# Optimization experiments

Measured on AMD Instinct MI355X. Metric: run time of the kernel, lower is better.

Reference implementation:

```python
import jax, jax.numpy as jnp
import numpy as np

N_NODES = 50000
N_EDGES = 600000
IN_CH = 128
OUT_CH = 128
HEADS = 1


def setup_inputs() -> dict:
    key = jax.random.key(0)
    ks = jax.random.split(key, 6)
    x = jax.random.normal(ks[0], (N_NODES, IN_CH), dtype=jnp.float32)
    edge_index = jax.random.randint(ks[1], (2, N_EDGES), 0, N_NODES, dtype=jnp.int64)
    weight = jax.random.normal(ks[2], (IN_CH, HEADS * OUT_CH), dtype=jnp.float32) * (1.0 / np.sqrt(IN_CH))
    u = jax.random.normal(ks[3], (IN_CH, HEADS), dtype=jnp.float32) * (1.0 / np.sqrt(IN_CH))
    c = jax.random.normal(ks[4], (HEADS,), dtype=jnp.float32)
    bias = jax.random.normal(ks[5], (OUT_CH,), dtype=jnp.float32) * 0.01
    return {"x": x, "edge_index": edge_index, "weight": weight, "u": u, "c": c, "bias": bias}


def reference(x, edge_index, weight, u, c, bias):
    N = x.shape[0]
    # FeaStConv default add_self_loops=True
    loops = jnp.arange(N, dtype=edge_index.dtype)
    src = jnp.concatenate([edge_index[0], loops])  # x_j (source / neighbor)
    dst = jnp.concatenate([edge_index[1], loops])  # x_i (target / center)
    # per-edge soft assignment over heads: q = softmax((x_j - x_i) @ u + c)
    q = jax.nn.softmax((x[src] - x[dst]) @ u + c, axis=1)          # [E, H]
    xj = (x[src] @ weight).reshape(-1, HEADS, OUT_CH)              # [E, H, F]
    msg = (xj * q[:, :, None]).sum(axis=1)                         # [E, F]
    # mean aggregation over incoming edges at each target node
    agg = jax.ops.segment_sum(msg, dst, num_segments=N)
    cnt = jax.ops.segment_sum(jnp.ones((dst.shape[0],), x.dtype), dst, num_segments=N)
    out = agg / jnp.maximum(cnt, 1.0)[:, None] + bias
    return jax.nn.relu(out)
```

## Files before the change

### kernel.cpp

```cpp
#include <hip/hip_runtime.h>

#define N_NODES 50000
#define N_EDGES 600000
#define CH 128
#define ROWS 32
#define MD 32
#define SPILL_CAP 65536
#define HSTRIDE 136

typedef __attribute__((ext_vector_type(8))) short bf16x8;
typedef __attribute__((ext_vector_type(4))) float f32x4;

__device__ inline unsigned int f2bf(float f) {
    unsigned int b = __float_as_uint(f);
    unsigned int r = b + 0x7fffu + ((b >> 16) & 1u);
    return r >> 16;
}

__device__ inline void acc8(float* a, int4 u) {
    a[0] += __uint_as_float(((unsigned int)u.x) << 16);
    a[1] += __uint_as_float(((unsigned int)u.x) & 0xffff0000u);
    a[2] += __uint_as_float(((unsigned int)u.y) << 16);
    a[3] += __uint_as_float(((unsigned int)u.y) & 0xffff0000u);
    a[4] += __uint_as_float(((unsigned int)u.z) << 16);
    a[5] += __uint_as_float(((unsigned int)u.z) & 0xffff0000u);
    a[6] += __uint_as_float(((unsigned int)u.w) << 16);
    a[7] += __uint_as_float(((unsigned int)u.w) & 0xffff0000u);
}

__global__ __launch_bounds__(256) void k_prep(const float* __restrict__ x,
                                              const float* __restrict__ Wm,
                                              unsigned short* __restrict__ xh,
                                              unsigned short* __restrict__ Wt,
                                              int* __restrict__ deg, int degN,
                                              int* __restrict__ spill_cnt) {
    int i = blockIdx.x * 256 + threadIdx.x;
    const int NX4 = N_NODES * CH / 4;
    if (i < NX4) {
        float4 v = ((const float4*)x)[i];
        ushort4 o;
        o.x = (unsigned short)f2bf(v.x);
        o.y = (unsigned short)f2bf(v.y);
        o.z = (unsigned short)f2bf(v.z);
        o.w = (unsigned short)f2bf(v.w);
        ((ushort4*)xh)[i] = o;
    }
    if (i < degN / 4) ((int4*)deg)[i] = make_int4(0, 0, 0, 0);
    if (i < CH * CH) {
        int n = i >> 7, k = i & 127;
        Wt[n * CH + k] = (unsigned short)f2bf(Wm[k * CH + n]);
    }
    if (i == 0) *spill_cnt = 0;
}

__global__ __launch_bounds__(256) void k_histfill(const int* __restrict__ ei,
                                                  int* __restrict__ deg, int pad,
                                                  int* __restrict__ ell,
                                                  int* __restrict__ spill_cnt,
                                                  int* __restrict__ spill) {
    int idx = blockIdx.x * 256 + threadIdx.x;
    if (idx * 4 >= N_EDGES) return;
    int4 s = ((const int4*)ei)[idx];
    int4 d = ((const int4*)(ei + N_EDGES))[idx];
    #pragma unroll
    for (int q = 0; q < 4; ++q) {
        int src = (q == 0) ? s.x : (q == 1) ? s.y : (q == 2) ? s.z : s.w;
        int dst = (q == 0) ? d.x : (q == 1) ? d.y : (q == 2) ? d.z : d.w;
        int r = atomicAdd(&deg[dst * pad], 1);
        if (r < MD) {
            ell[dst * MD + r] = src;
        } else {
            int p = atomicAdd(spill_cnt, 1);
            if (p < SPILL_CAP) {
                spill[2 * p] = src;
                spill[2 * p + 1] = dst;
            }
        }
    }
}

__global__ __launch_bounds__(256) void k_agg_mfma(
    const unsigned short* __restrict__ xh, const int* __restrict__ deg, int pad,
    const int* __restrict__ ell, const int* __restrict__ spill_cnt,
    const int* __restrict__ spill, const unsigned short* __restrict__ Wt,
    const float* __restrict__ bias, float* __restrict__ out) {
    __shared__ __align__(16) unsigned short HsB[ROWS * HSTRIDE];
    const int t = threadIdx.x;
    const int wv = t >> 6;
    const int lane = t & 63;
    const int quad = lane >> 4;
    const int l16 = lane & 15;
    const int row0 = blockIdx.x * ROWS;
    const int c8 = l16 * 8;

    #pragma unroll
    for (int kk = 0; kk < 2; ++kk) {
        const int ln = wv * 8 + kk * 4 + quad;
        const int n = row0 + ln;
        float a[8] = {0.f, 0.f, 0.f, 0.f, 0.f, 0.f, 0.f, 0.f};
        float inv = 1.0f;
        if (n < N_NODES) {
            acc8(a, *(const int4*)(xh + (size_t)n * CH + c8));
            const int d = deg[n * pad];
            const int dl = (d < MD) ? d : MD;
            const int* cl = ell + (size_t)n * MD;
            int j = 0;
            for (; j + 3 < dl; j += 4) {
                int e0 = cl[j], e1 = cl[j + 1], e2 = cl[j + 2], e3 = cl[j + 3];
                int4 u0 = *(const int4*)(xh + (size_t)e0 * CH + c8);
                int4 u1 = *(const int4*)(xh + (size_t)e1 * CH + c8);
                int4 u2 = *(const int4*)(xh + (size_t)e2 * CH + c8);
                int4 u3 = *(const int4*)(xh + (size_t)e3 * CH + c8);
                acc8(a, u0); acc8(a, u1); acc8(a, u2); acc8(a, u3);
            }
            for (; j < dl; ++j)
                acc8(a, *(const int4*)(xh + (size_t)cl[j] * CH + c8));
            int sc = *spill_cnt;
            if (sc > SPILL_CAP) sc = SPILL_CAP;
            for (int sidx = 0; sidx < sc; ++sidx) {
                if (spill[2 * sidx + 1] == n)
                    acc8(a, *(const int4*)(xh + (size_t)spill[2 * sidx] * CH + c8));
            }
            inv = 1.0f / (float)(d + 1);
        }
        int4 p;
        p.x = (int)(f2bf(a[0] * inv) | (f2bf(a[1] * inv) << 16));
        p.y = (int)(f2bf(a[2] * inv) | (f2bf(a[3] * inv) << 16));
        p.z = (int)(f2bf(a[4] * inv) | (f2bf(a[5] * inv) << 16));
        p.w = (int)(f2bf(a[6] * inv) | (f2bf(a[7] * inv) << 16));
        *(int4*)&HsB[ln * HSTRIDE + c8] = p;
    }
    __syncthreads();

    const int rt = wv >> 1;
    const int cstart = (wv & 1) * 64;
    f32x4 acc[4];
    #pragma unroll
    for (int tt = 0; tt < 4; ++tt) acc[tt] = (f32x4){0.f, 0.f, 0.f, 0.f};

    const unsigned short* hrow = &HsB[(rt * 16 + l16) * HSTRIDE + quad * 8];
    #pragma unroll
    for (int ks = 0; ks < 4; ++ks) {
        bf16x8 af = *(const bf16x8*)(hrow + ks * 32);
        #pragma unroll
        for (int tt = 0; tt < 4; ++tt) {
            const int ncol = cstart + tt * 16 + l16;
            bf16x8 bf = *(const bf16x8*)(Wt + (size_t)ncol * CH + ks * 32 + quad * 8);
            acc[tt] = __builtin_amdgcn_mfma_f32_16x16x32_bf16(af, bf, acc[tt], 0, 0, 0);
        }
    }

    #pragma unroll
    for (int tt = 0; tt < 4; ++tt) {
        const int ncol = cstart + tt * 16 + l16;
        const float bv = bias[ncol];
        #pragma unroll
        for (int r = 0; r < 4; ++r) {
            const int row = row0 + rt * 16 + quad * 4 + r;
            if (row < N_NODES)
                out[(size_t)row * CH + ncol] = fmaxf(acc[tt][r] + bv, 0.f);
        }
    }
}

extern "C" void kernel_launch(void* const* d_in, const int* in_sizes, int n_in,
                              void* d_out, int out_size, void* d_ws, size_t ws_size,
                              hipStream_t stream) {
    const float* x    = (const float*)d_in[0];
    const int*   ei   = (const int*)d_in[1];
    const float* Wm   = (const float*)d_in[2];
    const float* bias = (const float*)d_in[5];
    float* out = (float*)d_out;

    const size_t xh_bytes   = (size_t)N_NODES * CH * 2;
    const size_t wt_bytes   = (size_t)CH * CH * 2;
    const size_t ell_bytes  = (size_t)N_NODES * MD * 4;
    const size_t spill_bytes = (size_t)(1 + 2 * SPILL_CAP) * 4;
    const size_t fixed = xh_bytes + wt_bytes + ell_bytes + spill_bytes;

    int pad = 1;
    if (ws_size >= fixed + (size_t)N_NODES * 32 * 4) pad = 32;
    else if (ws_size >= fixed + (size_t)N_NODES * 8 * 4) pad = 8;
    const int degN = ((N_NODES * pad + 3) / 4) * 4;

    unsigned short* xh = (unsigned short*)d_ws;
    unsigned short* Wt = (unsigned short*)((char*)d_ws + xh_bytes);
    int* ell       = (int*)((char*)d_ws + xh_bytes + wt_bytes);
    int* spill_cnt = ell + (size_t)N_NODES * MD;
    int* spill     = spill_cnt + 1;
    int* deg       = spill + 2 * SPILL_CAP;

    k_prep<<<dim3((N_NODES * CH / 4 + 255) / 256), dim3(256), 0, stream>>>(
        x, Wm, xh, Wt, deg, degN, spill_cnt);
    k_histfill<<<dim3((N_EDGES / 4 + 255) / 256), dim3(256), 0, stream>>>(
        ei, deg, pad, ell, spill_cnt, spill);
    k_agg_mfma<<<dim3((N_NODES + ROWS - 1) / ROWS), dim3(256), 0, stream>>>(
        xh, deg, pad, ell, spill_cnt, spill, Wt, bias, out);
}
```

Measured before the change: 163.5 us.

## Fuse prep and histogram kernels, use 16-bit ELL, interleave two-node gathers

Merges the bf16 conversion and the edge histogram/ELL fill into one launch split by block index, with the degree and spill counters zeroed by a memset. The ELL neighbour list is stored as 16-bit indices to halve index traffic. The aggregation loop now gathers two nodes' neighbours together so more independent loads are in flight, and it skips the spill scan when no edges spilled. The 16-bit indices cannot hold source ids at or above 65536; with 50000 nodes they fit. Running the histogram concurrently with the conversion drops the dependency the old separate launch gave, so it relies on the histogram not reading xh.

```diff
diff --git a/kernel.cpp b/kernel.cpp
--- a/kernel.cpp
+++ b/kernel.cpp
@@ -7,6 +7,8 @@
 #define MD 32
 #define SPILL_CAP 65536
 #define HSTRIDE 136
+#define PREP_BLOCKS 6250
+#define HIST_BLOCKS 586
 
 typedef __attribute__((ext_vector_type(8))) short bf16x8;
 typedef __attribute__((ext_vector_type(4))) float f32x4;
@@ -28,15 +30,16 @@
     a[7] += __uint_as_float(((unsigned int)u.w) & 0xffff0000u);
 }
 
-__global__ __launch_bounds__(256) void k_prep(const float* __restrict__ x,
-                                              const float* __restrict__ Wm,
-                                              unsigned short* __restrict__ xh,
-                                              unsigned short* __restrict__ Wt,
-                                              int* __restrict__ deg, int degN,
-                                              int* __restrict__ spill_cnt) {
-    int i = blockIdx.x * 256 + threadIdx.x;
-    const int NX4 = N_NODES * CH / 4;
-    if (i < NX4) {
+__global__ __launch_bounds__(256) void k_prep_hist(
+    const float* __restrict__ x, const float* __restrict__ Wm,
+    const int* __restrict__ ei, unsigned short* __restrict__ xh,
+    unsigned short* __restrict__ Wt, unsigned short* __restrict__ ellu,
+    int* __restrict__ deg, int pad, int* __restrict__ spill_cnt,
+    int* __restrict__ spill) {
+    const int b = blockIdx.x;
+    const int t = threadIdx.x;
+    if (b < PREP_BLOCKS) {
+        int i = b * 256 + t;
         float4 v = ((const float4*)x)[i];
         ushort4 o;
         o.x = (unsigned short)f2bf(v.x);
@@ -44,36 +47,28 @@
         o.z = (unsigned short)f2bf(v.z);
         o.w = (unsigned short)f2bf(v.w);
         ((ushort4*)xh)[i] = o;
-    }
-    if (i < degN / 4) ((int4*)deg)[i] = make_int4(0, 0, 0, 0);
-    if (i < CH * CH) {
-        int n = i >> 7, k = i & 127;
-        Wt[n * CH + k] = (unsigned short)f2bf(Wm[k * CH + n]);
-    }
-    if (i == 0) *spill_cnt = 0;
-}
-
-__global__ __launch_bounds__(256) void k_histfill(const int* __restrict__ ei,
-                                                  int* __restrict__ deg, int pad,
-                                                  int* __restrict__ ell,
-                                                  int* __restrict__ spill_cnt,
-                                                  int* __restrict__ spill) {
-    int idx = blockIdx.x * 256 + threadIdx.x;
-    if (idx * 4 >= N_EDGES) return;
-    int4 s = ((const int4*)ei)[idx];
-    int4 d = ((const int4*)(ei + N_EDGES))[idx];
-    #pragma unroll
-    for (int q = 0; q < 4; ++q) {
-        int src = (q == 0) ? s.x : (q == 1) ? s.y : (q == 2) ? s.z : s.w;
-        int dst = (q == 0) ? d.x : (q == 1) ? d.y : (q == 2) ? d.z : d.w;
-        int r = atomicAdd(&deg[dst * pad], 1);
-        if (r < MD) {
-            ell[dst * MD + r] = src;
-        } else {
-            int p = atomicAdd(spill_cnt, 1);
-            if (p < SPILL_CAP) {
-                spill[2 * p] = src;
-                spill[2 * p + 1] = dst;
+        if (i < CH * CH) {
+            int n = i >> 7, k = i & 127;
+            Wt[n * CH + k] = (unsigned short)f2bf(Wm[k * CH + n]);
+        }
+    } else {
+        int idx = (b - PREP_BLOCKS) * 256 + t;
+        if (idx * 4 >= N_EDGES) return;
+        int4 s = ((const int4*)ei)[idx];
+        int4 d = ((const int4*)(ei + N_EDGES))[idx];
+        #pragma unroll
+        for (int q = 0; q < 4; ++q) {
+            int src = (q == 0) ? s.x : (q == 1) ? s.y : (q == 2) ? s.z : s.w;
+            int dst = (q == 0) ? d.x : (q == 1) ? d.y : (q == 2) ? d.z : d.w;
+            int r = atomicAdd(&deg[dst * pad], 1);
+            if (r < MD) {
+                ellu[dst * MD + r] = (unsigned short)src;
+            } else {
+                int p = atomicAdd(spill_cnt, 1);
+                if (p < SPILL_CAP) {
+                    spill[2 * p] = src;
+                    spill[2 * p + 1] = dst;
+                }
             }
         }
     }
@@ -81,7 +76,7 @@
 
 __global__ __launch_bounds__(256) void k_agg_mfma(
     const unsigned short* __restrict__ xh, const int* __restrict__ deg, int pad,
-    const int* __restrict__ ell, const int* __restrict__ spill_cnt,
+    const unsigned short* __restrict__ ellu, const int* __restrict__ spill_cnt,
     const int* __restrict__ spill, const unsigned short* __restrict__ Wt,
     const float* __restrict__ bias, float* __restrict__ out) {
     __shared__ __align__(16) unsigned short HsB[ROWS * HSTRIDE];
@@ -93,42 +88,77 @@
     const int row0 = blockIdx.x * ROWS;
     const int c8 = l16 * 8;
 
-    #pragma unroll
-    for (int kk = 0; kk < 2; ++kk) {
-        const int ln = wv * 8 + kk * 4 + quad;
-        const int n = row0 + ln;
-        float a[8] = {0.f, 0.f, 0.f, 0.f, 0.f, 0.f, 0.f, 0.f};
-        float inv = 1.0f;
-        if (n < N_NODES) {
-            acc8(a, *(const int4*)(xh + (size_t)n * CH + c8));
-            const int d = deg[n * pad];
-            const int dl = (d < MD) ? d : MD;
-            const int* cl = ell + (size_t)n * MD;
-            int j = 0;
-            for (; j + 3 < dl; j += 4) {
-                int e0 = cl[j], e1 = cl[j + 1], e2 = cl[j + 2], e3 = cl[j + 3];
-                int4 u0 = *(const int4*)(xh + (size_t)e0 * CH + c8);
-                int4 u1 = *(const int4*)(xh + (size_t)e1 * CH + c8);
-                int4 u2 = *(const int4*)(xh + (size_t)e2 * CH + c8);
-                int4 u3 = *(const int4*)(xh + (size_t)e3 * CH + c8);
-                acc8(a, u0); acc8(a, u1); acc8(a, u2); acc8(a, u3);
-            }
-            for (; j < dl; ++j)
-                acc8(a, *(const int4*)(xh + (size_t)cl[j] * CH + c8));
-            int sc = *spill_cnt;
+    {
+        const int lnA = wv * 8 + quad;
+        const int lnB = lnA + 4;
+        const int nA = row0 + lnA;
+        const int nB = row0 + lnB;
+        float a[8] = {}, bacc[8] = {};
+        int dA = 0, dB = 0;
+        if (nA < N_NODES) {
+            acc8(a, *(const int4*)(xh + (size_t)nA * CH + c8));
+            dA = deg[nA * pad];
+        }
+        if (nB < N_NODES) {
+            acc8(bacc, *(const int4*)(xh + (size_t)nB * CH + c8));
+            dB = deg[nB * pad];
+        }
+        const int dlA = (dA < MD) ? dA : MD;
+        const int dlB = (dB < MD) ? dB : MD;
+        const unsigned short* clA = ellu + (size_t)nA * MD;
+        const unsigned short* clB = ellu + (size_t)nB * MD;
+        const int dmax = (dlA > dlB) ? dlA : dlB;
+
+        for (int j = 0; j < dmax; j += 4) {
+            ushort4 cA = make_ushort4(0, 0, 0, 0), cB = make_ushort4(0, 0, 0, 0);
+            if (j < dlA) cA = *(const ushort4*)(clA + j);
+            if (j < dlB) cB = *(const ushort4*)(clB + j);
+            int4 uA0, uA1, uA2, uA3, uB0, uB1, uB2, uB3;
+            bool pA0 = j + 0 < dlA, pA1 = j + 1 < dlA, pA2 = j + 2 < dlA, pA3 = j + 3 < dlA;
+            bool pB0 = j + 0 < dlB, pB1 = j + 1 < dlB, pB2 = j + 2 < dlB, pB3 = j + 3 < dlB;
+            if (pA0) uA0 = *(const int4*)(xh + (size_t)cA.x * CH + c8);
+            if (pA1) uA1 = *(const int4*)(xh + (size_t)cA.y * CH + c8);
+            if (pA2) uA2 = *(const int4*)(xh + (size_t)cA.z * CH + c8);
+            if (pA3) uA3 = *(const int4*)(xh + (size_t)cA.w * CH + c8);
+            if (pB0) uB0 = *(const int4*)(xh + (size_t)cB.x * CH + c8);
+            if (pB1) uB1 = *(const int4*)(xh + (size_t)cB.y * CH + c8);
+            if (pB2) uB2 = *(const int4*)(xh + (size_t)cB.z * CH + c8);
+            if (pB3) uB3 = *(const int4*)(xh + (size_t)cB.w * CH + c8);
+            if (pA0) acc8(a, uA0);
+            if (pA1) acc8(a, uA1);
+            if (pA2) acc8(a, uA2);
+            if (pA3) acc8(a, uA3);
+            if (pB0) acc8(bacc, uB0);
+            if (pB1) acc8(bacc, uB1);
+            if (pB2) acc8(bacc, uB2);
+            if (pB3) acc8(bacc, uB3);
+        }
+
+        int sc = *spill_cnt;
+        if (sc > 0) {
             if (sc > SPILL_CAP) sc = SPILL_CAP;
             for (int sidx = 0; sidx < sc; ++sidx) {
-                if (spill[2 * sidx + 1] == n)
+                int sdst = spill[2 * sidx + 1];
+                if (sdst == nA)
                     acc8(a, *(const int4*)(xh + (size_t)spill[2 * sidx] * CH + c8));
+                if (sdst == nB)
+                    acc8(bacc, *(const int4*)(xh + (size_t)spill[2 * sidx] * CH + c8));
             }
-            inv = 1.0f / (float)(d + 1);
-        }
+        }
+
+        const float invA = 1.0f / (float)(dA + 1);
+        const float invB = 1.0f / (float)(dB + 1);
         int4 p;
-        p.x = (int)(f2bf(a[0] * inv) | (f2bf(a[1] * inv) << 16));
-        p.y = (int)(f2bf(a[2] * inv) | (f2bf(a[3] * inv) << 16));
-        p.z = (int)(f2bf(a[4] * inv) | (f2bf(a[5] * inv) << 16));
-        p.w = (int)(f2bf(a[6] * inv) | (f2bf(a[7] * inv) << 16));
-        *(int4*)&HsB[ln * HSTRIDE + c8] = p;
+        p.x = (int)(f2bf(a[0] * invA) | (f2bf(a[1] * invA) << 16));
+        p.y = (int)(f2bf(a[2] * invA) | (f2bf(a[3] * invA) << 16));
+        p.z = (int)(f2bf(a[4] * invA) | (f2bf(a[5] * invA) << 16));
+        p.w = (int)(f2bf(a[6] * invA) | (f2bf(a[7] * invA) << 16));
+        *(int4*)&HsB[lnA * HSTRIDE + c8] = p;
+        p.x = (int)(f2bf(bacc[0] * invB) | (f2bf(bacc[1] * invB) << 16));
+        p.y = (int)(f2bf(bacc[2] * invB) | (f2bf(bacc[3] * invB) << 16));
+        p.z = (int)(f2bf(bacc[4] * invB) | (f2bf(bacc[5] * invB) << 16));
+        p.w = (int)(f2bf(bacc[6] * invB) | (f2bf(bacc[7] * invB) << 16));
+        *(int4*)&HsB[lnB * HSTRIDE + c8] = p;
     }
     __syncthreads();
 
@@ -172,9 +202,9 @@
     const float* bias = (const float*)d_in[5];
     float* out = (float*)d_out;
 
-    const size_t xh_bytes   = (size_t)N_NODES * CH * 2;
-    const size_t wt_bytes   = (size_t)CH * CH * 2;
-    const size_t ell_bytes  = (size_t)N_NODES * MD * 4;
+    const size_t xh_bytes  = (size_t)N_NODES * CH * 2;
+    const size_t wt_bytes  = (size_t)CH * CH * 2;
+    const size_t ell_bytes = (size_t)N_NODES * MD * 2;
     const size_t spill_bytes = (size_t)(1 + 2 * SPILL_CAP) * 4;
     const size_t fixed = xh_bytes + wt_bytes + ell_bytes + spill_bytes;
 
@@ -183,17 +213,16 @@
     else if (ws_size >= fixed + (size_t)N_NODES * 8 * 4) pad = 8;
     const int degN = ((N_NODES * pad + 3) / 4) * 4;
 
-    unsigned short* xh = (unsigned short*)d_ws;
-    unsigned short* Wt = (unsigned short*)((char*)d_ws + xh_bytes);
-    int* ell       = (int*)((char*)d_ws + xh_bytes + wt_bytes);
-    int* spill_cnt = ell + (size_t)N_NODES * MD;
+    unsigned short* xh   = (unsigned short*)d_ws;
+    unsigned short* Wt   = (unsigned short*)((char*)d_ws + xh_bytes);
+    unsigned short* ellu = (unsigned short*)((char*)d_ws + xh_bytes + wt_bytes);
+    int* deg       = (int*)((char*)d_ws + xh_bytes + wt_bytes + ell_bytes);
+    int* spill_cnt = deg + degN;
     int* spill     = spill_cnt + 1;
-    int* deg       = spill + 2 * SPILL_CAP;
-
-    k_prep<<<dim3((N_NODES * CH / 4 + 255) / 256), dim3(256), 0, stream>>>(
-        x, Wm, xh, Wt, deg, degN, spill_cnt);
-    k_histfill<<<dim3((N_EDGES / 4 + 255) / 256), dim3(256), 0, stream>>>(
-        ei, deg, pad, ell, spill_cnt, spill);
+
+    hipMemsetAsync(deg, 0, (size_t)degN * 4 + 4, stream);
+    k_prep_hist<<<dim3(PREP_BLOCKS + HIST_BLOCKS), dim3(256), 0, stream>>>(
+        x, Wm, ei, xh, Wt, ellu, deg, pad, spill_cnt, spill);
     k_agg_mfma<<<dim3((N_NODES + ROWS - 1) / ROWS), dim3(256), 0, stream>>>(
-        xh, deg, pad, ell, spill_cnt, spill, Wt, bias, out);
-}
+        xh, deg, pad, ellu, spill_cnt, spill, Wt, bias, out);
+}
```

Measured after the change: 175.4 us. 1.07x slower.

## Merge prep and histogram kernels into one launch and halve aggregation tile rows

Applied to the files above, without the earlier changes.

The bf16 conversion of x and W and the edge-to-ELL histogram fill now run as disjoint block ranges of a single kernel. The degree array and spill counter are zeroed beforehand by one hipMemsetAsync. This removes a kernel boundary and lets the two independent prep phases overlap. The aggregation kernel now handles 16 rows per block, so each wave does one node and a 32-column MFMA slice, which doubles the block count. It also drops bounds checks and skips the spill scan when no edges spilled, at the cost of more per-block reloads of the weight matrix.

```diff
diff --git a/kernel.cpp b/kernel.cpp
--- a/kernel.cpp
+++ b/kernel.cpp
@@ -3,10 +3,12 @@
 #define N_NODES 50000
 #define N_EDGES 600000
 #define CH 128
-#define ROWS 32
+#define ROWS 16
 #define MD 32
 #define SPILL_CAP 65536
 #define HSTRIDE 136
+#define PREP_BLOCKS 6250
+#define HIST_BLOCKS 586
 
 typedef __attribute__((ext_vector_type(8))) short bf16x8;
 typedef __attribute__((ext_vector_type(4))) float f32x4;
@@ -28,15 +30,16 @@
     a[7] += __uint_as_float(((unsigned int)u.w) & 0xffff0000u);
 }
 
-__global__ __launch_bounds__(256) void k_prep(const float* __restrict__ x,
-                                              const float* __restrict__ Wm,
-                                              unsigned short* __restrict__ xh,
-                                              unsigned short* __restrict__ Wt,
-                                              int* __restrict__ deg, int degN,
-                                              int* __restrict__ spill_cnt) {
-    int i = blockIdx.x * 256 + threadIdx.x;
-    const int NX4 = N_NODES * CH / 4;
-    if (i < NX4) {
+__global__ __launch_bounds__(256) void k_prep_hist(
+    const float* __restrict__ x, const float* __restrict__ Wm,
+    const int* __restrict__ ei, unsigned short* __restrict__ xh,
+    unsigned short* __restrict__ Wt, int* __restrict__ ell,
+    int* __restrict__ deg, int pad, int* __restrict__ spill_cnt,
+    int* __restrict__ spill) {
+    const int b = blockIdx.x;
+    const int t = threadIdx.x;
+    if (b < PREP_BLOCKS) {
+        int i = b * 256 + t;
         float4 v = ((const float4*)x)[i];
         ushort4 o;
         o.x = (unsigned short)f2bf(v.x);
@@ -44,36 +47,28 @@
         o.z = (unsigned short)f2bf(v.z);
         o.w = (unsigned short)f2bf(v.w);
         ((ushort4*)xh)[i] = o;
-    }
-    if (i < degN / 4) ((int4*)deg)[i] = make_int4(0, 0, 0, 0);
-    if (i < CH * CH) {
-        int n = i >> 7, k = i & 127;
-        Wt[n * CH + k] = (unsigned short)f2bf(Wm[k * CH + n]);
-    }
-    if (i == 0) *spill_cnt = 0;
-}
-
-__global__ __launch_bounds__(256) void k_histfill(const int* __restrict__ ei,
-                                                  int* __restrict__ deg, int pad,
-                                                  int* __restrict__ ell,
-                                                  int* __restrict__ spill_cnt,
-                                                  int* __restrict__ spill) {
-    int idx = blockIdx.x * 256 + threadIdx.x;
-    if (idx * 4 >= N_EDGES) return;
-    int4 s = ((const int4*)ei)[idx];
-    int4 d = ((const int4*)(ei + N_EDGES))[idx];
-    #pragma unroll
-    for (int q = 0; q < 4; ++q) {
-        int src = (q == 0) ? s.x : (q == 1) ? s.y : (q == 2) ? s.z : s.w;
-        int dst = (q == 0) ? d.x : (q == 1) ? d.y : (q == 2) ? d.z : d.w;
-        int r = atomicAdd(&deg[dst * pad], 1);
-        if (r < MD) {
-            ell[dst * MD + r] = src;
-        } else {
-            int p = atomicAdd(spill_cnt, 1);
-            if (p < SPILL_CAP) {
-                spill[2 * p] = src;
-                spill[2 * p + 1] = dst;
+        if (i < CH * CH) {
+            int n = i >> 7, k = i & 127;
+            Wt[n * CH + k] = (unsigned short)f2bf(Wm[k * CH + n]);
+        }
+    } else {
+        int idx = (b - PREP_BLOCKS) * 256 + t;
+        if (idx * 4 >= N_EDGES) return;
+        int4 s = ((const int4*)ei)[idx];
+        int4 d = ((const int4*)(ei + N_EDGES))[idx];
+        #pragma unroll
+        for (int q = 0; q < 4; ++q) {
+            int src = (q == 0) ? s.x : (q == 1) ? s.y : (q == 2) ? s.z : s.w;
+            int dst = (q == 0) ? d.x : (q == 1) ? d.y : (q == 2) ? d.z : d.w;
+            int r = atomicAdd(&deg[dst * pad], 1);
+            if (r < MD) {
+                ell[dst * MD + r] = src;
+            } else {
+                int p = atomicAdd(spill_cnt, 1);
+                if (p < SPILL_CAP) {
+                    spill[2 * p] = src;
+                    spill[2 * p + 1] = dst;
+                }
             }
         }
     }
@@ -93,36 +88,34 @@
     const int row0 = blockIdx.x * ROWS;
     const int c8 = l16 * 8;
 
-    #pragma unroll
-    for (int kk = 0; kk < 2; ++kk) {
-        const int ln = wv * 8 + kk * 4 + quad;
+    {
+        const int ln = wv * 4 + quad;
         const int n = row0 + ln;
         float a[8] = {0.f, 0.f, 0.f, 0.f, 0.f, 0.f, 0.f, 0.f};
-        float inv = 1.0f;
-        if (n < N_NODES) {
-            acc8(a, *(const int4*)(xh + (size_t)n * CH + c8));
-            const int d = deg[n * pad];
-            const int dl = (d < MD) ? d : MD;
-            const int* cl = ell + (size_t)n * MD;
-            int j = 0;
-            for (; j + 3 < dl; j += 4) {
-                int e0 = cl[j], e1 = cl[j + 1], e2 = cl[j + 2], e3 = cl[j + 3];
-                int4 u0 = *(const int4*)(xh + (size_t)e0 * CH + c8);
-                int4 u1 = *(const int4*)(xh + (size_t)e1 * CH + c8);
-                int4 u2 = *(const int4*)(xh + (size_t)e2 * CH + c8);
-                int4 u3 = *(const int4*)(xh + (size_t)e3 * CH + c8);
-                acc8(a, u0); acc8(a, u1); acc8(a, u2); acc8(a, u3);
-            }
-            for (; j < dl; ++j)
-                acc8(a, *(const int4*)(xh + (size_t)cl[j] * CH + c8));
-            int sc = *spill_cnt;
+        acc8(a, *(const int4*)(xh + (size_t)n * CH + c8));
+        const int d = deg[n * pad];
+        const int dl = (d < MD) ? d : MD;
+        const int* cl = ell + (size_t)n * MD;
+        int j = 0;
+        for (; j + 3 < dl; j += 4) {
+            int e0 = cl[j], e1 = cl[j + 1], e2 = cl[j + 2], e3 = cl[j + 3];
+            int4 u0 = *(const int4*)(xh + (size_t)e0 * CH + c8);
+            int4 u1 = *(const int4*)(xh + (size_t)e1 * CH + c8);
+            int4 u2 = *(const int4*)(xh + (size_t)e2 * CH + c8);
+            int4 u3 = *(const int4*)(xh + (size_t)e3 * CH + c8);
+            acc8(a, u0); acc8(a, u1); acc8(a, u2); acc8(a, u3);
+        }
+        for (; j < dl; ++j)
+            acc8(a, *(const int4*)(xh + (size_t)cl[j] * CH + c8));
+        int sc = *spill_cnt;
+        if (sc > 0) {
             if (sc > SPILL_CAP) sc = SPILL_CAP;
             for (int sidx = 0; sidx < sc; ++sidx) {
                 if (spill[2 * sidx + 1] == n)
                     acc8(a, *(const int4*)(xh + (size_t)spill[2 * sidx] * CH + c8));
             }
-            inv = 1.0f / (float)(d + 1);
         }
+        const float inv = 1.0f / (float)(d + 1);
         int4 p;
         p.x = (int)(f2bf(a[0] * inv) | (f2bf(a[1] * inv) << 16));
         p.y = (int)(f2bf(a[2] * inv) | (f2bf(a[3] * inv) << 16));
@@ -132,33 +125,30 @@
     }
     __syncthreads();
 
-    const int rt = wv >> 1;
-    const int cstart = (wv & 1) * 64;
-    f32x4 acc[4];
-    #pragma unroll
-    for (int tt = 0; tt < 4; ++tt) acc[tt] = (f32x4){0.f, 0.f, 0.f, 0.f};
+    f32x4 acc[2];
+    acc[0] = (f32x4){0.f, 0.f, 0.f, 0.f};
+    acc[1] = (f32x4){0.f, 0.f, 0.f, 0.f};
 
-    const unsigned short* hrow = &HsB[(rt * 16 + l16) * HSTRIDE + quad * 8];
+    const unsigned short* hrow = &HsB[l16 * HSTRIDE + quad * 8];
     #pragma unroll
     for (int ks = 0; ks < 4; ++ks) {
         bf16x8 af = *(const bf16x8*)(hrow + ks * 32);
         #pragma unroll
-        for (int tt = 0; tt < 4; ++tt) {
-            const int ncol = cstart + tt * 16 + l16;
+        for (int tt = 0; tt < 2; ++tt) {
+            const int ncol = wv * 32 + tt * 16 + l16;
             bf16x8 bf = *(const bf16x8*)(Wt + (size_t)ncol * CH + ks * 32 + quad * 8);
             acc[tt] = __builtin_amdgcn_mfma_f32_16x16x32_bf16(af, bf, acc[tt], 0, 0, 0);
         }
     }
 
     #pragma unroll
-    for (int tt = 0; tt < 4; ++tt) {
-        const int ncol = cstart + tt * 16 + l16;
+    for (int tt = 0; tt < 2; ++tt) {
+        const int ncol = wv * 32 + tt * 16 + l16;
         const float bv = bias[ncol];
         #pragma unroll
         for (int r = 0; r < 4; ++r) {
-            const int row = row0 + rt * 16 + quad * 4 + r;
-            if (row < N_NODES)
-                out[(size_t)row * CH + ncol] = fmaxf(acc[tt][r] + bv, 0.f);
+            const int row = row0 + quad * 4 + r;
+            out[(size_t)row * CH + ncol] = fmaxf(acc[tt][r] + bv, 0.f);
         }
     }
 }
@@ -172,9 +162,9 @@
     const float* bias = (const float*)d_in[5];
     float* out = (float*)d_out;
 
-    const size_t xh_bytes   = (size_t)N_NODES * CH * 2;
-    const size_t wt_bytes   = (size_t)CH * CH * 2;
-    const size_t ell_bytes  = (size_t)N_NODES * MD * 4;
+    const size_t xh_bytes  = (size_t)N_NODES * CH * 2;
+    const size_t wt_bytes  = (size_t)CH * CH * 2;
+    const size_t ell_bytes = (size_t)N_NODES * MD * 4;
     const size_t spill_bytes = (size_t)(1 + 2 * SPILL_CAP) * 4;
     const size_t fixed = xh_bytes + wt_bytes + ell_bytes + spill_bytes;
 
@@ -186,14 +176,13 @@
     unsigned short* xh = (unsigned short*)d_ws;
     unsigned short* Wt = (unsigned short*)((char*)d_ws + xh_bytes);
     int* ell       = (int*)((char*)d_ws + xh_bytes + wt_bytes);
-    int* spill_cnt = ell + (size_t)N_NODES * MD;
+    int* deg       = ell + (size_t)N_NODES * MD;
+    int* spill_cnt = deg + degN;
     int* spill     = spill_cnt + 1;
-    int* deg       = spill + 2 * SPILL_CAP;
 
-    k_prep<<<dim3((N_NODES * CH / 4 + 255) / 256), dim3(256), 0, stream>>>(
-        x, Wm, xh, Wt, deg, degN, spill_cnt);
-    k_histfill<<<dim3((N_EDGES / 4 + 255) / 256), dim3(256), 0, stream>>>(
-        ei, deg, pad, ell, spill_cnt, spill);
-    k_agg_mfma<<<dim3((N_NODES + ROWS - 1) / ROWS), dim3(256), 0, stream>>>(
+    hipMemsetAsync(deg, 0, (size_t)degN * 4 + 4, stream);
+    k_prep_hist<<<dim3(PREP_BLOCKS + HIST_BLOCKS), dim3(256), 0, stream>>>(
+        x, Wm, ei, xh, Wt, ell, deg, pad, spill_cnt, spill);
+    k_agg_mfma<<<dim3(N_NODES / ROWS), dim3(256), 0, stream>>>(
         xh, deg, pad, ell, spill_cnt, spill, Wt, bias, out);
 }
```

Result: faster. 157.8 us (-3.5%).
